# Kernel tuning notes

Hardware: AMD Instinct MI355X
Metric: run time of the kernel (lower is better)

The kernel has to match this reference:

```python
import jax, jax.numpy as jnp
import numpy as np

N = 10000      # nodes
E = 160000     # edges (before self-loops)
H = 4          # heads
C = 256        # per-head channels
D_IN = 512
D_OUT = 512
NEG_SLOPE = 0.2  # PyG GATConv default negative_slope


def gat_conv(x, src, dst, W, a_src, a_dst, bias):
    """PyG-style GATConv with concat=True. x:[n,d_in], W:[d_in,H*C]."""
    n = x.shape[0]
    h = (x @ W).reshape(n, H, C)                       # [n,H,C]
    al_s = jnp.einsum('nhc,hc->nh', h, a_src)          # [n,H]
    al_d = jnp.einsum('nhc,hc->nh', h, a_dst)          # [n,H]
    e = jax.nn.leaky_relu(al_s[src] + al_d[dst], NEG_SLOPE)   # [Etot,H]
    # segment softmax over edges grouped by destination node
    emax = jax.ops.segment_max(e, dst, num_segments=n)
    w = jnp.exp(e - emax[dst])
    denom = jax.ops.segment_sum(w, dst, num_segments=n)
    alpha = w / denom[dst]                             # [Etot,H]
    out = jax.ops.segment_sum(h[src] * alpha[:, :, None], dst, num_segments=n)
    return out.reshape(n, H * C) + bias


def setup_inputs() -> dict:
    key = jax.random.key(0)
    ks = jax.random.split(key, 13)
    s = 0.05
    return {
        'x': jax.random.normal(ks[0], (N, D_IN), jnp.float32),
        'edge_index': jax.random.randint(ks[1], (2, E), 0, N, dtype=jnp.int32),
        'W1': jax.random.normal(ks[2], (D_IN, H * C), jnp.float32) * s,
        'a_src1': jax.random.normal(ks[3], (H, C), jnp.float32) * s,
        'a_dst1': jax.random.normal(ks[4], (H, C), jnp.float32) * s,
        'b1': jnp.zeros((H * C,), jnp.float32),
        'W2': jax.random.normal(ks[5], (H * C, H * C), jnp.float32) * s,
        'a_src2': jax.random.normal(ks[6], (H, C), jnp.float32) * s,
        'a_dst2': jax.random.normal(ks[7], (H, C), jnp.float32) * s,
        'b2': jnp.zeros((H * C,), jnp.float32),
        'Wfc': jax.random.normal(ks[8], (H * C, D_OUT), jnp.float32) * s,
        'bfc': jnp.zeros((D_OUT,), jnp.float32),
    }


def reference(x, edge_index, W1, a_src1, a_dst1, b1, W2, a_src2, a_dst2, b2, Wfc, bfc):
    # PyG GATConv default add_self_loops=True
    loop = jnp.arange(N, dtype=edge_index.dtype)
    src = jnp.concatenate([edge_index[0], loop])
    dst = jnp.concatenate([edge_index[1], loop])
    h = jax.nn.relu(gat_conv(x, src, dst, W1, a_src1, a_dst1, b1))
    # dropout is identity in eval mode
    h = jax.nn.relu(gat_conv(h, src, dst, W2, a_src2, a_dst2, b2))
    return h @ Wfc + bfc
```

## Files before the change

kernel.cpp:

```cpp
#include <hip/hip_runtime.h>

#define NND 10000
#define NED 160000
#define NET 170000
#define MP  10112
#define DH  1024
#define DIN 512
#define DOUT 512
#define CHUNK 128

typedef unsigned short u16;
typedef __attribute__((ext_vector_type(8))) short short8_t;
typedef __attribute__((ext_vector_type(4))) float f32x4_t;

__device__ __forceinline__ u16 f2bf(float f) {
  unsigned u = __float_as_uint(f);
  return (u16)((u + 0x7fffu + ((u >> 16) & 1u)) >> 16);
}
__device__ __forceinline__ float bf2f(u16 b) {
  return __uint_as_float(((unsigned)b) << 16);
}
__device__ __forceinline__ float bflo(unsigned u) { return __uint_as_float(u << 16); }
__device__ __forceinline__ float bfhi(unsigned u) { return __uint_as_float(u & 0xffff0000u); }
__device__ __forceinline__ float lrelu(float v) { return v > 0.f ? v : 0.2f * v; }

__device__ __forceinline__ void gl_lds16(const void* g, void* l) {
  __builtin_amdgcn_global_load_lds(
      (const __attribute__((address_space(1))) unsigned int*)g,
      (__attribute__((address_space(3))) unsigned int*)l, 16, 0, 0);
}


__global__ void k_prep0(int* __restrict__ indeg, int* __restrict__ cursor,
                        u16* __restrict__ hbp, u16* __restrict__ h2bp) {
  int i = blockIdx.x * 256 + threadIdx.x;
  if (i < NND) { indeg[i] = 0; cursor[i] = 0; }
  const uint4 z = make_uint4(0, 0, 0, 0);
  if (i < (MP - NND) * DH / 8) {
    ((uint4*)hbp)[i] = z;
    ((uint4*)h2bp)[i] = z;
  }
}

__global__ void k_conv_x(const float* __restrict__ x, u16* __restrict__ xb) {
  int i = blockIdx.x * 256 + threadIdx.x;
  const int total = MP * DIN / 4;
  if (i >= total) return;
  float4 v = make_float4(0.f, 0.f, 0.f, 0.f);
  if (i < NND * DIN / 4) v = ((const float4*)x)[i];
  ushort4 o;
  o.x = f2bf(v.x); o.y = f2bf(v.y); o.z = f2bf(v.z); o.w = f2bf(v.w);
  ((ushort4*)xb)[i] = o;
}

__global__ void k_transpose_w(const float* __restrict__ W, u16* __restrict__ WT,
                              int K, int Nt) {
  __shared__ float s[32][33];
  int kt = blockIdx.y * 32, nt = blockIdx.x * 32;
  int tx = threadIdx.x, ty = threadIdx.y;
#pragma unroll
  for (int i = 0; i < 32; i += 8)
    s[ty + i][tx] = W[(size_t)(kt + ty + i) * Nt + nt + tx];
  __syncthreads();
#pragma unroll
  for (int i = 0; i < 32; i += 8)
    WT[(size_t)(nt + ty + i) * K + kt + tx] = f2bf(s[tx][ty + i]);
}


__global__ void k_count(const int* __restrict__ ei, int* __restrict__ indeg) {
  int e = blockIdx.x * 256 + threadIdx.x;
  if (e >= NET) return;
  int dst = (e < NED) ? ei[NED + e] : (e - NED);
  atomicAdd(&indeg[dst], 1);
}

__global__ void k_scan(const int* __restrict__ indeg, int* __restrict__ rowp) {
  __shared__ int wsum[16];
  __shared__ int carry_s;
  const int t = threadIdx.x, wv = t >> 6, ln = t & 63;
  if (t == 0) { carry_s = 0; rowp[0] = 0; }
  __syncthreads();
  for (int base = 0; base < NND; base += 1024) {
    int v = (base + t < NND) ? indeg[base + t] : 0;
    int sc = v;
#pragma unroll
    for (int off = 1; off < 64; off <<= 1) {
      int xx = __shfl_up(sc, off);
      if (ln >= off) sc += xx;
    }
    if (ln == 63) wsum[wv] = sc;
    __syncthreads();
    if (t < 16) {
      int ws = wsum[t];
#pragma unroll
      for (int off = 1; off < 16; off <<= 1) {
        int xx = __shfl_up(ws, off);
        if (ln >= off) ws += xx;
      }
      wsum[t] = ws;
    }
    __syncthreads();
    int add = carry_s + (wv ? wsum[wv - 1] : 0);
    if (base + t < NND) rowp[base + t + 1] = sc + add;
    int tot = wsum[15];
    __syncthreads();
    if (t == 0) carry_s += tot;
    __syncthreads();
  }
}

__global__ void k_fill(const int* __restrict__ ei, const int* __restrict__ rowp,
                       int* __restrict__ cursor, int* __restrict__ colsrc) {
  int e = blockIdx.x * 256 + threadIdx.x;
  if (e >= NET) return;
  int src, dst;
  if (e < NED) { src = ei[e]; dst = ei[NED + e]; }
  else         { src = dst = e - NED; }
  int pos = rowp[dst] + atomicAdd(&cursor[dst], 1);
  colsrc[pos] = src;
}


template <int KD, int GX, bool HAS_BIAS, bool GUARD, bool OUTBF>
__global__ __launch_bounds__(256) void k_gemm(const u16* __restrict__ A,
                                              const u16* __restrict__ BT,
                                              float* __restrict__ Cf,
                                              u16* __restrict__ Cb,
                                              const float* __restrict__ bias,
                                              int ldc, int mvalid) {
  __shared__ __align__(16) u16 As[128 * 32];
  __shared__ __align__(16) u16 Bs[128 * 32];
  const int tid = threadIdx.x;
  const int lane = tid & 63;
  const int w = tid >> 6;
  const int wr = w >> 1, wc = w & 1;
  const int l15 = lane & 15;
  const int kg = (lane >> 4) * 8;

  const int nwg = GX * gridDim.y;
  const int bid = blockIdx.y * GX + blockIdx.x;
  const int q = nwg >> 3, r = nwg & 7;
  const int xcd = bid & 7, idx = bid >> 3;
  const int swz = (xcd < r ? xcd * (q + 1) : r * (q + 1) + (xcd - r) * q) + idx;
  const int mt = swz / GX, nt = swz % GX;

  const int flat0 = tid * 8;
  const int row0 = flat0 >> 5, kk0 = flat0 & 31;
  const int row1 = 64 + row0;

  const u16* Ab = A + (size_t)(mt * 128) * KD;
  const u16* Bb = BT + (size_t)(nt * 128) * KD;
  const u16* ga0 = Ab + row0 * KD + kk0;
  const u16* ga1 = Ab + row1 * KD + kk0;
  const u16* gb0 = Bb + row0 * KD + kk0;
  const u16* gb1 = Bb + row1 * KD + kk0;
  u16* lA0 = As + flat0;
  u16* lA1 = As + 2048 + flat0;
  u16* lB0 = Bs + flat0;
  u16* lB1 = Bs + 2048 + flat0;

  f32x4_t acc[4][4];
#pragma unroll
  for (int i = 0; i < 4; i++)
#pragma unroll
    for (int j = 0; j < 4; j++)
#pragma unroll
      for (int q2 = 0; q2 < 4; q2++) acc[i][j][q2] = 0.f;

  for (int kt = 0; kt < KD; kt += 32) {
    __syncthreads();
    gl_lds16(ga0 + kt, lA0);
    gl_lds16(ga1 + kt, lA1);
    gl_lds16(gb0 + kt, lB0);
    gl_lds16(gb1 + kt, lB1);
    __syncthreads();
    short8_t af[4], bfr[4];
#pragma unroll
    for (int i = 0; i < 4; i++)
      af[i] = *(const short8_t*)(As + (wr * 64 + i * 16 + l15) * 32 + kg);
#pragma unroll
    for (int i = 0; i < 4; i++)
      bfr[i] = *(const short8_t*)(Bs + (wc * 64 + i * 16 + l15) * 32 + kg);
#pragma unroll
    for (int i = 0; i < 4; i++)
#pragma unroll
      for (int j = 0; j < 4; j++)
        acc[i][j] = __builtin_amdgcn_mfma_f32_16x16x32_bf16(af[i], bfr[j], acc[i][j], 0, 0, 0);
  }

  const int rbase = mt * 128 + wr * 64 + (lane >> 4) * 4;
  const int cbase = nt * 128 + wc * 64 + l15;
#pragma unroll
  for (int i = 0; i < 4; i++) {
#pragma unroll
    for (int j = 0; j < 4; j++) {
#pragma unroll
      for (int q2 = 0; q2 < 4; q2++) {
        int rr = rbase + i * 16 + q2;
        int cc = cbase + j * 16;
        if (!GUARD || rr < mvalid) {
          float v = acc[i][j][q2];
          if (HAS_BIAS) v += bias[cc];
          if (OUTBF) Cb[(size_t)rr * ldc + cc] = f2bf(v);
          else       Cf[(size_t)rr * ldc + cc] = v;
        }
      }
    }
  }
}


__global__ __launch_bounds__(256) void k_al(const u16* __restrict__ hprojb,
                                            const float* __restrict__ a_src,
                                            const float* __restrict__ a_dst,
                                            float* __restrict__ al_s,
                                            float* __restrict__ al_d) {
  int n = blockIdx.x, t = threadIdx.x;
  ushort4 hq = ((const ushort4*)(hprojb + (size_t)n * DH))[t];
  float4 as = ((const float4*)a_src)[t];
  float4 ad = ((const float4*)a_dst)[t];
  float hx = bf2f(hq.x), hy = bf2f(hq.y), hz = bf2f(hq.z), hw = bf2f(hq.w);
  float ps = hx * as.x + hy * as.y + hz * as.z + hw * as.w;
  float pd = hx * ad.x + hy * ad.y + hz * ad.z + hw * ad.w;
#pragma unroll
  for (int off = 32; off; off >>= 1) {
    ps += __shfl_xor(ps, off);
    pd += __shfl_xor(pd, off);
  }
  if ((t & 63) == 0) {
    int h = t >> 6;
    al_s[n * 4 + h] = ps;
    al_d[n * 4 + h] = pd;
  }
}


__global__ __launch_bounds__(256) void k_agg(const u16* __restrict__ hprojb,
                                             const float* __restrict__ al_s,
                                             const float* __restrict__ al_d,
                                             const int* __restrict__ rowp,
                                             const int* __restrict__ colsrc,
                                             const float* __restrict__ bias,
                                             u16* __restrict__ outb) {
  __shared__ int csrc[CHUNK];
  __shared__ float cw[CHUNK * 4];
  __shared__ float smax[4][4];
  __shared__ float sbmax[4];
  __shared__ float comb[128 * 9];
  const int n = blockIdx.x, t = threadIdx.x;
  const int wv = t >> 6, ln = t & 63;
  const int half = t >> 7, u = t & 127;
  const int head = u >> 5;
  const int beg = rowp[n], end = rowp[n + 1];
  const float4 ad = ((const float4*)al_d)[n];

  float m0 = -1e30f, m1 = -1e30f, m2 = -1e30f, m3 = -1e30f;
  for (int e = beg + t; e < end; e += 256) {
    int s = colsrc[e];
    float4 as = ((const float4*)al_s)[s];
    m0 = fmaxf(m0, lrelu(as.x + ad.x));
    m1 = fmaxf(m1, lrelu(as.y + ad.y));
    m2 = fmaxf(m2, lrelu(as.z + ad.z));
    m3 = fmaxf(m3, lrelu(as.w + ad.w));
  }
#pragma unroll
  for (int off = 32; off; off >>= 1) {
    m0 = fmaxf(m0, __shfl_xor(m0, off));
    m1 = fmaxf(m1, __shfl_xor(m1, off));
    m2 = fmaxf(m2, __shfl_xor(m2, off));
    m3 = fmaxf(m3, __shfl_xor(m3, off));
  }
  if (ln == 0) { smax[0][wv] = m0; smax[1][wv] = m1; smax[2][wv] = m2; smax[3][wv] = m3; }
  __syncthreads();
  if (t < 4)
    sbmax[t] = fmaxf(fmaxf(smax[t][0], smax[t][1]), fmaxf(smax[t][2], smax[t][3]));
  __syncthreads();
  const float bm0 = sbmax[0], bm1 = sbmax[1], bm2 = sbmax[2], bm3 = sbmax[3];

  float a0 = 0.f, a1 = 0.f, a2 = 0.f, a3 = 0.f;
  float a4 = 0.f, a5 = 0.f, a6 = 0.f, a7 = 0.f;
  float dsum = 0.f;
  const u16* hrow = hprojb + u * 8;
  for (int cs = beg; cs < end; cs += CHUNK) {
    int m = end - cs; if (m > CHUNK) m = CHUNK;
    __syncthreads();
    if (t < m) {
      int s = colsrc[cs + t];
      csrc[t] = s;
      float4 as = ((const float4*)al_s)[s];
      float4 wv4;
      wv4.x = __expf(lrelu(as.x + ad.x) - bm0);
      wv4.y = __expf(lrelu(as.y + ad.y) - bm1);
      wv4.z = __expf(lrelu(as.z + ad.z) - bm2);
      wv4.w = __expf(lrelu(as.w + ad.w) - bm3);
      ((float4*)cw)[t] = wv4;
    }
    __syncthreads();
    for (int i = half; i < m; i += 2) {
      int s = csrc[i];
      float wgt = cw[i * 4 + head];
      uint4 hv = *(const uint4*)(hrow + (size_t)s * DH);
      a0 += bflo(hv.x) * wgt; a1 += bfhi(hv.x) * wgt;
      a2 += bflo(hv.y) * wgt; a3 += bfhi(hv.y) * wgt;
      a4 += bflo(hv.z) * wgt; a5 += bfhi(hv.z) * wgt;
      a6 += bflo(hv.w) * wgt; a7 += bfhi(hv.w) * wgt;
      dsum += wgt;
    }
  }
  __syncthreads();
  if (half) {
    float* cb = comb + u * 9;
    cb[0] = a0; cb[1] = a1; cb[2] = a2; cb[3] = a3;
    cb[4] = a4; cb[5] = a5; cb[6] = a6; cb[7] = a7;
    cb[8] = dsum;
  }
  __syncthreads();
  if (!half) {
    const float* cb = comb + u * 9;
    a0 += cb[0]; a1 += cb[1]; a2 += cb[2]; a3 += cb[3];
    a4 += cb[4]; a5 += cb[5]; a6 += cb[6]; a7 += cb[7];
    dsum += cb[8];
    const float inv = 1.f / dsum;
    float4 bv0 = ((const float4*)bias)[u * 2];
    float4 bv1 = ((const float4*)bias)[u * 2 + 1];
    float o0 = fmaxf(a0 * inv + bv0.x, 0.f);
    float o1 = fmaxf(a1 * inv + bv0.y, 0.f);
    float o2 = fmaxf(a2 * inv + bv0.z, 0.f);
    float o3 = fmaxf(a3 * inv + bv0.w, 0.f);
    float o4 = fmaxf(a4 * inv + bv1.x, 0.f);
    float o5 = fmaxf(a5 * inv + bv1.y, 0.f);
    float o6 = fmaxf(a6 * inv + bv1.z, 0.f);
    float o7 = fmaxf(a7 * inv + bv1.w, 0.f);
    uint4 ob;
    ob.x = (unsigned)f2bf(o0) | ((unsigned)f2bf(o1) << 16);
    ob.y = (unsigned)f2bf(o2) | ((unsigned)f2bf(o3) << 16);
    ob.z = (unsigned)f2bf(o4) | ((unsigned)f2bf(o5) << 16);
    ob.w = (unsigned)f2bf(o6) | ((unsigned)f2bf(o7) << 16);
    ((uint4*)(outb + (size_t)n * DH))[u] = ob;
  }
}


extern "C" void kernel_launch(void* const* d_in, const int* in_sizes, int n_in,
                              void* d_out, int out_size, void* d_ws, size_t ws_size,
                              hipStream_t stream) {
  const float* x   = (const float*)d_in[0];
  const int*   ei  = (const int*)d_in[1];
  const float* W1  = (const float*)d_in[2];
  const float* as1 = (const float*)d_in[3];
  const float* ad1 = (const float*)d_in[4];
  const float* b1  = (const float*)d_in[5];
  const float* W2  = (const float*)d_in[6];
  const float* as2 = (const float*)d_in[7];
  const float* ad2 = (const float*)d_in[8];
  const float* b2  = (const float*)d_in[9];
  const float* Wfc = (const float*)d_in[10];
  const float* bfc = (const float*)d_in[11];
  float* out = (float*)d_out;
  (void)in_sizes; (void)n_in; (void)out_size; (void)ws_size;

  char* p = (char*)d_ws;
  auto carve = [&](size_t bytes) -> char* {
    char* r = p; p += (bytes + 255) & ~(size_t)255; return r;
  };
  u16*   xb     = (u16*)  carve((size_t)MP * DIN * 2);
  u16*   w1t    = (u16*)  carve((size_t)DH * DIN * 2);
  u16*   w2t    = (u16*)  carve((size_t)DH * DH * 2);
  u16*   wft    = (u16*)  carve((size_t)DOUT * DH * 2);
  u16*   hprojb = (u16*)  carve((size_t)MP * DH * 2);
  u16*   hb     = (u16*)  carve((size_t)MP * DH * 2);
  u16*   h2b    = (u16*)  carve((size_t)MP * DH * 2);
  float* als    = (float*)carve((size_t)NND * 4 * 4);
  float* ald    = (float*)carve((size_t)NND * 4 * 4);
  int*   indeg  = (int*)  carve((size_t)NND * 4);
  int*   rowp   = (int*)  carve((size_t)(NND + 1) * 4);
  int*   cursor = (int*)  carve((size_t)NND * 4);
  int*   colsrc = (int*)  carve((size_t)NET * 4);

  k_prep0<<<((MP - NND) * DH / 8 + 255) / 256, 256, 0, stream>>>(indeg, cursor,
      hb + (size_t)NND * DH, h2b + (size_t)NND * DH);
  k_conv_x<<<(MP * DIN / 4 + 255) / 256, 256, 0, stream>>>(x, xb);
  k_transpose_w<<<dim3(DH / 32, DIN / 32), dim3(32, 8), 0, stream>>>(W1, w1t, DIN, DH);
  k_transpose_w<<<dim3(DH / 32, DH / 32), dim3(32, 8), 0, stream>>>(W2, w2t, DH, DH);
  k_transpose_w<<<dim3(DOUT / 32, DH / 32), dim3(32, 8), 0, stream>>>(Wfc, wft, DH, DOUT);
  k_count<<<(NET + 255) / 256, 256, 0, stream>>>(ei, indeg);
  k_scan<<<1, 1024, 0, stream>>>(indeg, rowp);
  k_fill<<<(NET + 255) / 256, 256, 0, stream>>>(ei, rowp, cursor, colsrc);

  k_gemm<DIN, 8, false, false, true><<<dim3(DH / 128, MP / 128), 256, 0, stream>>>(xb, w1t, nullptr, hprojb, nullptr, DH, MP);
  k_al<<<NND, 256, 0, stream>>>(hprojb, as1, ad1, als, ald);
  k_agg<<<NND, 256, 0, stream>>>(hprojb, als, ald, rowp, colsrc, b1, hb);

  k_gemm<DH, 8, false, false, true><<<dim3(DH / 128, MP / 128), 256, 0, stream>>>(hb, w2t, nullptr, hprojb, nullptr, DH, MP);
  k_al<<<NND, 256, 0, stream>>>(hprojb, as2, ad2, als, ald);
  k_agg<<<NND, 256, 0, stream>>>(hprojb, als, ald, rowp, colsrc, b2, h2b);

  k_gemm<DH, 4, true, true, false><<<dim3(DOUT / 128, MP / 128), 256, 0, stream>>>(h2b, wft, out, nullptr, bfc, DOUT, NND);
}
```

Measured before the change: 244.3 us.

## Split GAT aggregation into softmax-weight kernel and wave-sized gather kernel; parallelize scan

```diff
diff --git a/kernel.cpp b/kernel.cpp
--- a/kernel.cpp
+++ b/kernel.cpp
@@ -7,7 +7,7 @@
 #define DH  1024
 #define DIN 512
 #define DOUT 512
-#define CHUNK 128
+#define SCB 40
 
 typedef unsigned short u16;
 typedef __attribute__((ext_vector_type(8))) short short8_t;
@@ -31,10 +31,10 @@
 }
 
 
-__global__ void k_prep0(int* __restrict__ indeg, int* __restrict__ cursor,
+__global__ void k_prep0(int* __restrict__ indeg,
                         u16* __restrict__ hbp, u16* __restrict__ h2bp) {
   int i = blockIdx.x * 256 + threadIdx.x;
-  if (i < NND) { indeg[i] = 0; cursor[i] = 0; }
+  if (i < NND) indeg[i] = 0;
   const uint4 z = make_uint4(0, 0, 0, 0);
   if (i < (MP - NND) * DH / 8) {
     ((uint4*)hbp)[i] = z;
@@ -75,39 +75,49 @@
   atomicAdd(&indeg[dst], 1);
 }
 
-__global__ void k_scan(const int* __restrict__ indeg, int* __restrict__ rowp) {
-  __shared__ int wsum[16];
-  __shared__ int carry_s;
-  const int t = threadIdx.x, wv = t >> 6, ln = t & 63;
-  if (t == 0) { carry_s = 0; rowp[0] = 0; }
+__global__ void k_scan1(const int* __restrict__ indeg, int* __restrict__ rowp,
+                        int* __restrict__ bsum) {
+  __shared__ int ws[4];
+  const int b = blockIdx.x, t = threadIdx.x, wv = t >> 6, ln = t & 63;
+  const int i = b * 256 + t;
+  int v = (i < NND) ? indeg[i] : 0;
+  int sc = v;
+#pragma unroll
+  for (int off = 1; off < 64; off <<= 1) {
+    int xx = __shfl_up(sc, off);
+    if (ln >= off) sc += xx;
+  }
+  if (ln == 63) ws[wv] = sc;
   __syncthreads();
-  for (int base = 0; base < NND; base += 1024) {
-    int v = (base + t < NND) ? indeg[base + t] : 0;
-    int sc = v;
-#pragma unroll
-    for (int off = 1; off < 64; off <<= 1) {
-      int xx = __shfl_up(sc, off);
-      if (ln >= off) sc += xx;
-    }
-    if (ln == 63) wsum[wv] = sc;
-    __syncthreads();
-    if (t < 16) {
-      int ws = wsum[t];
-#pragma unroll
-      for (int off = 1; off < 16; off <<= 1) {
-        int xx = __shfl_up(ws, off);
-        if (ln >= off) ws += xx;
-      }
-      wsum[t] = ws;
-    }
-    __syncthreads();
-    int add = carry_s + (wv ? wsum[wv - 1] : 0);
-    if (base + t < NND) rowp[base + t + 1] = sc + add;
-    int tot = wsum[15];
-    __syncthreads();
-    if (t == 0) carry_s += tot;
-    __syncthreads();
-  }
+  if (t == 0) {
+    int a = 0;
+#pragma unroll
+    for (int k = 0; k < 4; k++) { int tmp = ws[k]; ws[k] = a; a += tmp; }
+    bsum[b] = a;
+  }
+  __syncthreads();
+  sc += ws[wv];
+  if (i < NND) rowp[i + 1] = sc;
+}
+
+__global__ void k_scan2(int* __restrict__ bsum) {
+  int t = threadIdx.x;
+  int v = (t < SCB) ? bsum[t] : 0;
+  int sc = v;
+#pragma unroll
+  for (int off = 1; off < 64; off <<= 1) {
+    int xx = __shfl_up(sc, off);
+    if (t >= off) sc += xx;
+  }
+  if (t < SCB) bsum[t] = sc - v;
+}
+
+__global__ void k_scan3(int* __restrict__ rowp, const int* __restrict__ bsum,
+                        int* __restrict__ cursor) {
+  const int b = blockIdx.x, t = threadIdx.x;
+  const int i = b * 256 + t;
+  if (i < NND) { rowp[i + 1] += bsum[b]; cursor[i] = 0; }
+  if (i == 0) rowp[0] = 0;
 }
 
 __global__ void k_fill(const int* __restrict__ ei, const int* __restrict__ rowp,
@@ -236,27 +246,17 @@
 }
 
 
-__global__ __launch_bounds__(256) void k_agg(const u16* __restrict__ hprojb,
-                                             const float* __restrict__ al_s,
-                                             const float* __restrict__ al_d,
-                                             const int* __restrict__ rowp,
-                                             const int* __restrict__ colsrc,
-                                             const float* __restrict__ bias,
-                                             u16* __restrict__ outb) {
-  __shared__ int csrc[CHUNK];
-  __shared__ float cw[CHUNK * 4];
-  __shared__ float smax[4][4];
-  __shared__ float sbmax[4];
-  __shared__ float comb[128 * 9];
-  const int n = blockIdx.x, t = threadIdx.x;
-  const int wv = t >> 6, ln = t & 63;
-  const int half = t >> 7, u = t & 127;
-  const int head = u >> 5;
+__global__ __launch_bounds__(64) void k_alpha(const float* __restrict__ al_s,
+                                              const float* __restrict__ al_d,
+                                              const int* __restrict__ rowp,
+                                              const int* __restrict__ colsrc,
+                                              float* __restrict__ alpha) {
+  const int n = blockIdx.x, ln = threadIdx.x;
   const int beg = rowp[n], end = rowp[n + 1];
   const float4 ad = ((const float4*)al_d)[n];
 
   float m0 = -1e30f, m1 = -1e30f, m2 = -1e30f, m3 = -1e30f;
-  for (int e = beg + t; e < end; e += 256) {
+  for (int e = beg + ln; e < end; e += 64) {
     int s = colsrc[e];
     float4 as = ((const float4*)al_s)[s];
     m0 = fmaxf(m0, lrelu(as.x + ad.x));
@@ -271,74 +271,86 @@
     m2 = fmaxf(m2, __shfl_xor(m2, off));
     m3 = fmaxf(m3, __shfl_xor(m3, off));
   }
-  if (ln == 0) { smax[0][wv] = m0; smax[1][wv] = m1; smax[2][wv] = m2; smax[3][wv] = m3; }
-  __syncthreads();
-  if (t < 4)
-    sbmax[t] = fmaxf(fmaxf(smax[t][0], smax[t][1]), fmaxf(smax[t][2], smax[t][3]));
-  __syncthreads();
-  const float bm0 = sbmax[0], bm1 = sbmax[1], bm2 = sbmax[2], bm3 = sbmax[3];
+
+  float d0 = 0.f, d1 = 0.f, d2 = 0.f, d3 = 0.f;
+  for (int e = beg + ln; e < end; e += 64) {
+    int s = colsrc[e];
+    float4 as = ((const float4*)al_s)[s];
+    float4 wv;
+    wv.x = __expf(lrelu(as.x + ad.x) - m0);
+    wv.y = __expf(lrelu(as.y + ad.y) - m1);
+    wv.z = __expf(lrelu(as.z + ad.z) - m2);
+    wv.w = __expf(lrelu(as.w + ad.w) - m3);
+    ((float4*)alpha)[e] = wv;
+    d0 += wv.x; d1 += wv.y; d2 += wv.z; d3 += wv.w;
+  }
+#pragma unroll
+  for (int off = 32; off; off >>= 1) {
+    d0 += __shfl_xor(d0, off);
+    d1 += __shfl_xor(d1, off);
+    d2 += __shfl_xor(d2, off);
+    d3 += __shfl_xor(d3, off);
+  }
+  const float i0 = 1.f / d0, i1 = 1.f / d1, i2 = 1.f / d2, i3 = 1.f / d3;
+  for (int e = beg + ln; e < end; e += 64) {
+    float4 wv = ((const float4*)alpha)[e];
+    wv.x *= i0; wv.y *= i1; wv.z *= i2; wv.w *= i3;
+    ((float4*)alpha)[e] = wv;
+  }
+}
+
+
+__global__ __launch_bounds__(64) void k_agg2(const u16* __restrict__ hprojb,
+                                             const float* __restrict__ alpha,
+                                             const int* __restrict__ rowp,
+                                             const int* __restrict__ colsrc,
+                                             const float* __restrict__ bias,
+                                             u16* __restrict__ outb) {
+  const int n = blockIdx.x, half = blockIdx.y, ln = threadIdx.x;
+  const int beg = rowp[n], end = rowp[n + 1];
+  const int hsel = 2 * half + (ln >> 5);
+  const u16* hbase = hprojb + half * 512 + ln * 8;
 
   float a0 = 0.f, a1 = 0.f, a2 = 0.f, a3 = 0.f;
   float a4 = 0.f, a5 = 0.f, a6 = 0.f, a7 = 0.f;
-  float dsum = 0.f;
-  const u16* hrow = hprojb + u * 8;
-  for (int cs = beg; cs < end; cs += CHUNK) {
-    int m = end - cs; if (m > CHUNK) m = CHUNK;
-    __syncthreads();
-    if (t < m) {
-      int s = colsrc[cs + t];
-      csrc[t] = s;
-      float4 as = ((const float4*)al_s)[s];
-      float4 wv4;
-      wv4.x = __expf(lrelu(as.x + ad.x) - bm0);
-      wv4.y = __expf(lrelu(as.y + ad.y) - bm1);
-      wv4.z = __expf(lrelu(as.z + ad.z) - bm2);
-      wv4.w = __expf(lrelu(as.w + ad.w) - bm3);
-      ((float4*)cw)[t] = wv4;
-    }
-    __syncthreads();
-    for (int i = half; i < m; i += 2) {
-      int s = csrc[i];
-      float wgt = cw[i * 4 + head];
-      uint4 hv = *(const uint4*)(hrow + (size_t)s * DH);
-      a0 += bflo(hv.x) * wgt; a1 += bfhi(hv.x) * wgt;
-      a2 += bflo(hv.y) * wgt; a3 += bfhi(hv.y) * wgt;
-      a4 += bflo(hv.z) * wgt; a5 += bfhi(hv.z) * wgt;
-      a6 += bflo(hv.w) * wgt; a7 += bfhi(hv.w) * wgt;
-      dsum += wgt;
-    }
-  }
-  __syncthreads();
-  if (half) {
-    float* cb = comb + u * 9;
-    cb[0] = a0; cb[1] = a1; cb[2] = a2; cb[3] = a3;
-    cb[4] = a4; cb[5] = a5; cb[6] = a6; cb[7] = a7;
-    cb[8] = dsum;
-  }
-  __syncthreads();
-  if (!half) {
-    const float* cb = comb + u * 9;
-    a0 += cb[0]; a1 += cb[1]; a2 += cb[2]; a3 += cb[3];
-    a4 += cb[4]; a5 += cb[5]; a6 += cb[6]; a7 += cb[7];
-    dsum += cb[8];
-    const float inv = 1.f / dsum;
-    float4 bv0 = ((const float4*)bias)[u * 2];
-    float4 bv1 = ((const float4*)bias)[u * 2 + 1];
-    float o0 = fmaxf(a0 * inv + bv0.x, 0.f);
-    float o1 = fmaxf(a1 * inv + bv0.y, 0.f);
-    float o2 = fmaxf(a2 * inv + bv0.z, 0.f);
-    float o3 = fmaxf(a3 * inv + bv0.w, 0.f);
-    float o4 = fmaxf(a4 * inv + bv1.x, 0.f);
-    float o5 = fmaxf(a5 * inv + bv1.y, 0.f);
-    float o6 = fmaxf(a6 * inv + bv1.z, 0.f);
-    float o7 = fmaxf(a7 * inv + bv1.w, 0.f);
-    uint4 ob;
-    ob.x = (unsigned)f2bf(o0) | ((unsigned)f2bf(o1) << 16);
-    ob.y = (unsigned)f2bf(o2) | ((unsigned)f2bf(o3) << 16);
-    ob.z = (unsigned)f2bf(o4) | ((unsigned)f2bf(o5) << 16);
-    ob.w = (unsigned)f2bf(o6) | ((unsigned)f2bf(o7) << 16);
-    ((uint4*)(outb + (size_t)n * DH))[u] = ob;
-  }
+  int e = beg;
+  for (; e + 1 < end; e += 2) {
+    int s0 = colsrc[e], s1 = colsrc[e + 1];
+    float w0 = alpha[e * 4 + hsel];
+    float w1 = alpha[(e + 1) * 4 + hsel];
+    uint4 h0 = *(const uint4*)(hbase + (size_t)s0 * DH);
+    uint4 h1 = *(const uint4*)(hbase + (size_t)s1 * DH);
+    a0 += bflo(h0.x) * w0; a1 += bfhi(h0.x) * w0;
+    a2 += bflo(h0.y) * w0; a3 += bfhi(h0.y) * w0;
+    a4 += bflo(h0.z) * w0; a5 += bfhi(h0.z) * w0;
+    a6 += bflo(h0.w) * w0; a7 += bfhi(h0.w) * w0;
+    a0 += bflo(h1.x) * w1; a1 += bfhi(h1.x) * w1;
+    a2 += bflo(h1.y) * w1; a3 += bfhi(h1.y) * w1;
+    a4 += bflo(h1.z) * w1; a5 += bfhi(h1.z) * w1;
+    a6 += bflo(h1.w) * w1; a7 += bfhi(h1.w) * w1;
+  }
+  if (e < end) {
+    int s0 = colsrc[e];
+    float w0 = alpha[e * 4 + hsel];
+    uint4 h0 = *(const uint4*)(hbase + (size_t)s0 * DH);
+    a0 += bflo(h0.x) * w0; a1 += bfhi(h0.x) * w0;
+    a2 += bflo(h0.y) * w0; a3 += bfhi(h0.y) * w0;
+    a4 += bflo(h0.z) * w0; a5 += bfhi(h0.z) * w0;
+    a6 += bflo(h0.w) * w0; a7 += bfhi(h0.w) * w0;
+  }
+
+  const float4 bv0 = *(const float4*)(bias + half * 512 + ln * 8);
+  const float4 bv1 = *(const float4*)(bias + half * 512 + ln * 8 + 4);
+  float o0 = fmaxf(a0 + bv0.x, 0.f), o1 = fmaxf(a1 + bv0.y, 0.f);
+  float o2 = fmaxf(a2 + bv0.z, 0.f), o3 = fmaxf(a3 + bv0.w, 0.f);
+  float o4 = fmaxf(a4 + bv1.x, 0.f), o5 = fmaxf(a5 + bv1.y, 0.f);
+  float o6 = fmaxf(a6 + bv1.z, 0.f), o7 = fmaxf(a7 + bv1.w, 0.f);
+  uint4 ob;
+  ob.x = (unsigned)f2bf(o0) | ((unsigned)f2bf(o1) << 16);
+  ob.y = (unsigned)f2bf(o2) | ((unsigned)f2bf(o3) << 16);
+  ob.z = (unsigned)f2bf(o4) | ((unsigned)f2bf(o5) << 16);
+  ob.w = (unsigned)f2bf(o6) | ((unsigned)f2bf(o7) << 16);
+  *(uint4*)(outb + (size_t)n * DH + half * 512 + ln * 8) = ob;
 }
 
 
@@ -373,28 +385,34 @@
   u16*   h2b    = (u16*)  carve((size_t)MP * DH * 2);
   float* als    = (float*)carve((size_t)NND * 4 * 4);
   float* ald    = (float*)carve((size_t)NND * 4 * 4);
+  float* alpha  = (float*)carve((size_t)NET * 4 * 4);
   int*   indeg  = (int*)  carve((size_t)NND * 4);
   int*   rowp   = (int*)  carve((size_t)(NND + 1) * 4);
   int*   cursor = (int*)  carve((size_t)NND * 4);
   int*   colsrc = (int*)  carve((size_t)NET * 4);
-
-  k_prep0<<<((MP - NND) * DH / 8 + 255) / 256, 256, 0, stream>>>(indeg, cursor,
+  int*   bsum   = (int*)  carve((size_t)SCB * 4);
+
+  k_prep0<<<((MP - NND) * DH / 8 + 255) / 256, 256, 0, stream>>>(indeg,
       hb + (size_t)NND * DH, h2b + (size_t)NND * DH);
   k_conv_x<<<(MP * DIN / 4 + 255) / 256, 256, 0, stream>>>(x, xb);
   k_transpose_w<<<dim3(DH / 32, DIN / 32), dim3(32, 8), 0, stream>>>(W1, w1t, DIN, DH);
   k_transpose_w<<<dim3(DH / 32, DH / 32), dim3(32, 8), 0, stream>>>(W2, w2t, DH, DH);
   k_transpose_w<<<dim3(DOUT / 32, DH / 32), dim3(32, 8), 0, stream>>>(Wfc, wft, DH, DOUT);
   k_count<<<(NET + 255) / 256, 256, 0, stream>>>(ei, indeg);
-  k_scan<<<1, 1024, 0, stream>>>(indeg, rowp);
+  k_scan1<<<SCB, 256, 0, stream>>>(indeg, rowp, bsum);
+  k_scan2<<<1, 64, 0, stream>>>(bsum);
+  k_scan3<<<SCB, 256, 0, stream>>>(rowp, bsum, cursor);
   k_fill<<<(NET + 255) / 256, 256, 0, stream>>>(ei, rowp, cursor, colsrc);
 
   k_gemm<DIN, 8, false, false, true><<<dim3(DH / 128, MP / 128), 256, 0, stream>>>(xb, w1t, nullptr, hprojb, nullptr, DH, MP);
   k_al<<<NND, 256, 0, stream>>>(hprojb, as1, ad1, als, ald);
-  k_agg<<<NND, 256, 0, stream>>>(hprojb, als, ald, rowp, colsrc, b1, hb);
+  k_alpha<<<NND, 64, 0, stream>>>(als, ald, rowp, colsrc, alpha);
+  k_agg2<<<dim3(NND, 2), 64, 0, stream>>>(hprojb, alpha, rowp, colsrc, b1, hb);
 
   k_gemm<DH, 8, false, false, true><<<dim3(DH / 128, MP / 128), 256, 0, stream>>>(hb, w2t, nullptr, hprojb, nullptr, DH, MP);
   k_al<<<NND, 256, 0, stream>>>(hprojb, as2, ad2, als, ald);
-  k_agg<<<NND, 256, 0, stream>>>(hprojb, als, ald, rowp, colsrc, b2, h2b);
+  k_alpha<<<NND, 64, 0, stream>>>(als, ald, rowp, colsrc, alpha);
+  k_agg2<<<dim3(NND, 2), 64, 0, stream>>>(hprojb, alpha, rowp, colsrc, b2, h2b);
 
   k_gemm<DH, 4, true, true, false><<<dim3(DOUT / 128, MP / 128), 256, 0, stream>>>(h2b, wft, out, nullptr, bfc, DOUT, NND);
 }
```

Result: no change. 240.6 us (-1.5%).
